# Performance work log

Hardware: AMD Instinct MI355X
Metric: run time of the kernel (lower is better)

The kernel has to match this reference:

```python
import jax, jax.numpy as jnp
import numpy as np
from jax import lax

DN = ('NCHW', 'OIHW', 'NCHW')


def conv2d(x, w, b, stride, pad):
    y = lax.conv_general_dilated(x, w, (stride, stride), [(pad, pad), (pad, pad)],
                                 dimension_numbers=DN)
    return y + b[None, :, None, None]


def conv_transpose2d_k4s2p1(x, w, b):
    # torch ConvTranspose2d(k=4, s=2, p=1); w is torch layout [Cin, Cout, 4, 4].
    # Equivalent forward conv: lhs_dilation=2, pad = k-1-p = 2, spatially-flipped kernel.
    k = jnp.flip(w, (2, 3)).transpose(1, 0, 2, 3)  # -> OIHW [Cout, Cin, 4, 4]
    y = lax.conv_general_dilated(x, k, (1, 1), [(2, 2), (2, 2)],
                                 lhs_dilation=(2, 2), dimension_numbers=DN)
    return y + b[None, :, None, None]


def setup_inputs() -> dict:
    key = jax.random.key(0)
    ks = jax.random.split(key, 16)

    def w(k, shape):
        fan_in = int(np.prod(shape[1:]))
        return jax.random.normal(k, shape, jnp.float32) * np.float32(1.0 / np.sqrt(fan_in))

    inp = {}
    inp['x'] = jax.random.uniform(ks[0], (256, 1, 128, 128), jnp.float32)
    # Encoder
    inp['enc_w1'] = w(ks[1], (32, 1, 4, 4));   inp['enc_b1'] = jnp.zeros((32,), jnp.float32)
    inp['enc_w2'] = w(ks[2], (64, 32, 4, 4));  inp['enc_b2'] = jnp.zeros((64,), jnp.float32)
    inp['enc_w3'] = w(ks[3], (64, 64, 3, 3));  inp['enc_b3'] = jnp.zeros((64,), jnp.float32)
    inp['enc_w4'] = w(ks[4], (32, 64, 1, 1));  inp['enc_b4'] = jnp.zeros((32,), jnp.float32)
    # Codebook: uniform(-sqrt(3/512), sqrt(3/512))
    mx = np.float32(np.sqrt(3.0 / 512.0))
    inp['codebook'] = jax.random.uniform(ks[5], (512, 32), jnp.float32, -mx, mx)
    # Decoder
    inp['dec_w1'] = w(ks[6], (64, 32, 3, 3));  inp['dec_b1'] = jnp.zeros((64,), jnp.float32)
    inp['dect_w1'] = w(ks[7], (64, 32, 4, 4)); inp['dect_b1'] = jnp.zeros((32,), jnp.float32)  # torch [Cin,Cout,k,k]
    inp['dect_w2'] = w(ks[8], (32, 1, 4, 4));  inp['dect_b2'] = jnp.zeros((1,), jnp.float32)
    return inp


def vqvae_forward(x, enc_w1, enc_b1, enc_w2, enc_b2, enc_w3, enc_b3, enc_w4, enc_b4,
                  codebook, dec_w1, dec_b1, dect_w1, dect_b1, dect_w2, dect_b2):
    # Encoder: 128 -> 64 -> 32 spatial, 32 channels out
    h = jax.nn.relu(conv2d(x, enc_w1, enc_b1, 2, 1))
    h = jax.nn.relu(conv2d(h, enc_w2, enc_b2, 2, 1))
    h = jax.nn.relu(conv2d(h, enc_w3, enc_b3, 1, 1))
    z = conv2d(h, enc_w4, enc_b4, 1, 0)            # [B, 32, 32, 32]

    # Vector quantization (NCHW -> NHWC -> flat)
    zin = jnp.moveaxis(z, 1, -1)                   # [B, H, W, D]
    flat = zin.reshape(-1, zin.shape[-1])          # [N, D]
    dists = (jnp.sum(flat * flat, -1, keepdims=True)
             + jnp.sum(codebook * codebook, -1)
             - 2.0 * flat @ codebook.T)            # [N, K]
    idx = jnp.argmin(dists, -1)                    # [N]
    quant = codebook[idx].reshape(zin.shape)       # == one_hot @ codebook

    emb_loss = jnp.mean((quant - lax.stop_gradient(zin)) ** 2)
    com_loss = 0.26 * jnp.mean((lax.stop_gradient(quant) - zin) ** 2)
    vq_loss = emb_loss + com_loss
    quant = zin + lax.stop_gradient(quant - zin)   # straight-through
    qz = jnp.moveaxis(quant, -1, 1)                # [B, 32, 32, 32]

    # Decoder: 32 -> 64 -> 128 spatial
    d = jax.nn.relu(conv2d(qz, dec_w1, dec_b1, 1, 1))
    d = jax.nn.relu(conv_transpose2d_k4s2p1(d, dect_w1, dect_b1))
    recon = jax.nn.sigmoid(conv_transpose2d_k4s2p1(d, dect_w2, dect_b2))
    return recon, vq_loss


def reference(x, enc_w1, enc_b1, enc_w2, enc_b2, enc_w3, enc_b3, enc_w4, enc_b4,
              codebook, dec_w1, dec_b1, dect_w1, dect_b1, dect_w2, dect_b2):
    return vqvae_forward(x, enc_w1, enc_b1, enc_w2, enc_b2, enc_w3, enc_b3, enc_w4, enc_b4,
                         codebook, dec_w1, dec_b1, dect_w1, dect_b1, dect_w2, dect_b2)
```

## Files before the change

kernel.cpp:

```cpp
#include <hip/hip_runtime.h>
#include <math.h>

typedef __attribute__((ext_vector_type(8))) short short8;
typedef __attribute__((ext_vector_type(4))) float f32x4;

__device__ inline unsigned short f2bf(float f) {
  unsigned u = __float_as_uint(f);
  u = (u + 0x7fffu + ((u >> 16) & 1u)) >> 16;
  return (unsigned short)u;
}

__global__ __launch_bounds__(256, 4)
void conv1_lds(const float* __restrict__ x, const float* __restrict__ w,
               const float* __restrict__ bias, float* __restrict__ out) {
  int bid = blockIdx.x;
  int cchunk = bid & 1;
  int t4 = (bid >> 1) & 3;
  int n = bid >> 3;
  int co0 = cchunk * 16;
  int y0 = t4 * 16;
  int yi0 = 2 * y0 - 1;

  __shared__ float xs[34 * 128];
  __shared__ float wl[16][16];

  int t = threadIdx.x;
  for (int idx = t; idx < 34 * 128; idx += 256) {
    int gy = yi0 + (idx >> 7);
    int gx = idx & 127;
    bool ok = (unsigned)gy < 128;
    xs[idx] = ok ? x[(size_t)n * 16384 + gy * 128 + gx] : 0.f;
  }
  {
    int cc = t & 15;
    int tap = t >> 4;
    if (t < 256) wl[tap][cc] = w[(size_t)(co0 + cc) * 16 + tap];
  }
  __syncthreads();

  int sx = t & 63;
  int rg = t >> 6;

  float acc[4][16];
#pragma unroll
  for (int j = 0; j < 4; j++)
#pragma unroll
    for (int c = 0; c < 16; c++) acc[j][c] = 0.f;

  int ix0 = 2 * sx - 1;
#pragma unroll
  for (int ky = 0; ky < 4; ky++) {
#pragma unroll
    for (int kx = 0; kx < 4; kx++) {
      int ix = ix0 + kx;
      bool xok = (unsigned)ix < 128;
      float xv[4];
#pragma unroll
      for (int j = 0; j < 4; j++) {
        int lrow = 2 * (4 * rg + j) + ky;
        float v = xs[lrow * 128 + (xok ? ix : 0)];
        xv[j] = xok ? v : 0.f;
      }
      const float* wr = &wl[ky * 4 + kx][0];
#pragma unroll
      for (int c = 0; c < 16; c += 4) {
        float4 wv = *(const float4*)(wr + c);
#pragma unroll
        for (int j = 0; j < 4; j++) {
          acc[j][c + 0] = fmaf(xv[j], wv.x, acc[j][c + 0]);
          acc[j][c + 1] = fmaf(xv[j], wv.y, acc[j][c + 1]);
          acc[j][c + 2] = fmaf(xv[j], wv.z, acc[j][c + 2]);
          acc[j][c + 3] = fmaf(xv[j], wv.w, acc[j][c + 3]);
        }
      }
    }
  }

#pragma unroll
  for (int j = 0; j < 4; j++) {
    int oy = y0 + 4 * rg + j;
    float* op = out + (((size_t)n * 32 + co0) * 64 + oy) * 64 + sx;
#pragma unroll
    for (int c = 0; c < 16; c++) {
      float v = acc[j][c] + bias[co0 + c];
      op[(size_t)c * 4096] = fmaxf(v, 0.f);
    }
  }
}

template<int CIN, int COUT, int CCH>
__global__ __launch_bounds__(256, 4)
void conv4x4s2_p(const float* __restrict__ x, const float* __restrict__ w,
                 const float* __restrict__ bias, float* __restrict__ out) {
  constexpr int NCH = COUT / CCH;
  int bid = blockIdx.x;
  int cchunk = bid % NCH;
  int n = bid / NCH;
  int co0 = cchunk * CCH;

  __shared__ float xs[66 * 68];
  __shared__ float wl[16][CCH];

  int t = threadIdx.x;
  int sx = t & 31;
  int sy0 = t >> 5;

  for (int i = t; i < 66 * 68; i += 256) xs[i] = 0.f;

  float acc[4][CCH];
#pragma unroll
  for (int j = 0; j < 4; j++)
#pragma unroll
    for (int c = 0; c < CCH; c++) acc[j][c] = 0.f;

  const float* xn = x + (size_t)n * CIN * 4096;

  for (int ci = 0; ci < CIN; ci++) {
    __syncthreads();
#pragma unroll
    for (int k = 0; k < 4; k++) {
      int idx = k * 1024 + t * 4;
      int row = idx >> 6;
      int col = idx & 63;
      float4 v = *(const float4*)(xn + (size_t)ci * 4096 + idx);
      float* rp = xs + (row + 1) * 68;
      int h = col >> 1;
      rp[34 + h]     = v.x;
      rp[h + 1]      = v.y;
      rp[34 + h + 1] = v.z;
      rp[h + 2]      = v.w;
    }
    {
      int cc = t & (CCH - 1);
      int tap = t >> 4;
      if (tap < 16) wl[tap][cc] = w[(size_t)(co0 + cc) * (CIN * 16) + ci * 16 + tap];
    }
    __syncthreads();

#pragma unroll
    for (int ky = 0; ky < 4; ky++) {
#pragma unroll
      for (int kx = 0; kx < 4; kx++) {
        int pc = ((kx & 1) ? 34 : 0) + sx + (kx >> 1);
        float xv[4];
#pragma unroll
        for (int j = 0; j < 4; j++) {
          int row = 2 * (sy0 + j * 8) + ky;
          xv[j] = xs[row * 68 + pc];
        }
        const float* wr = &wl[ky * 4 + kx][0];
#pragma unroll
        for (int c = 0; c < CCH; c += 4) {
          float4 wv = *(const float4*)(wr + c);
#pragma unroll
          for (int j = 0; j < 4; j++) {
            acc[j][c + 0] = fmaf(xv[j], wv.x, acc[j][c + 0]);
            acc[j][c + 1] = fmaf(xv[j], wv.y, acc[j][c + 1]);
            acc[j][c + 2] = fmaf(xv[j], wv.z, acc[j][c + 2]);
            acc[j][c + 3] = fmaf(xv[j], wv.w, acc[j][c + 3]);
          }
        }
      }
    }
  }

#pragma unroll
  for (int j = 0; j < 4; j++) {
    int sy = sy0 + j * 8;
    float* op = out + (((size_t)n * COUT + co0) * 32 + sy) * 32 + sx;
#pragma unroll
    for (int c = 0; c < CCH; c++) {
      float v = acc[j][c] + bias[co0 + c];
      v = fmaxf(v, 0.f);
      op[(size_t)c * 1024] = v;
    }
  }
}

template<int CIN, int COUT>
__global__ __launch_bounds__(256, 3)
void conv3x3_r8(const float* __restrict__ x, const float* __restrict__ w,
                const float* __restrict__ bias, float* __restrict__ out) {
  constexpr int NCH = COUT / 16;
  int bid = blockIdx.x;
  int cchunk = bid % NCH;
  int n = bid / NCH;
  int co0 = cchunk * 16;

  __shared__ float xs[4 * 34 * 34];
  __shared__ float wl[4 * 9][16];

  int t = threadIdx.x;
  int sx = t & 31;
  int rg = (t >> 5) & 3;
  int cob = (t >> 7) * 8;

  for (int i = t; i < 4 * 34 * 34; i += 256) xs[i] = 0.f;

  float acc[8][8];
#pragma unroll
  for (int j = 0; j < 8; j++)
#pragma unroll
    for (int c = 0; c < 8; c++) acc[j][c] = 0.f;

  const float* xn = x + (size_t)n * CIN * 1024;

  for (int cg = 0; cg < CIN / 4; cg++) {
    __syncthreads();
#pragma unroll
    for (int k = 0; k < 4; k++) {
      int row = t >> 3;
      int col = (t & 7) * 4;
      float4 v = *(const float4*)(xn + (size_t)(cg * 4 + k) * 1024 + t * 4);
      float* dst = xs + k * 1156 + (row + 1) * 34 + col + 1;
      dst[0] = v.x; dst[1] = v.y; dst[2] = v.z; dst[3] = v.w;
    }
    for (int i = t; i < 4 * 9 * 16; i += 256) {
      int cc = i & 15;
      int row = i >> 4;
      int c4 = row / 9, kk = row % 9;
      wl[row][cc] = w[(size_t)(co0 + cc) * (CIN * 9) + (cg * 4 + c4) * 9 + kk];
    }
    __syncthreads();

#pragma unroll
    for (int c4 = 0; c4 < 4; c4++) {
      const float* xc = xs + c4 * 1156;
      float xv[10][3];
#pragma unroll
      for (int r = 0; r < 10; r++) {
#pragma unroll
        for (int cx = 0; cx < 3; cx++)
          xv[r][cx] = xc[(8 * rg + r) * 34 + sx + cx];
      }
#pragma unroll
      for (int ky = 0; ky < 3; ky++) {
#pragma unroll
        for (int kx = 0; kx < 3; kx++) {
          const float* wr = &wl[c4 * 9 + ky * 3 + kx][cob];
          float4 w0 = *(const float4*)(wr);
          float4 w1 = *(const float4*)(wr + 4);
#pragma unroll
          for (int j = 0; j < 8; j++) {
            float xx = xv[j + ky][kx];
            acc[j][0] = fmaf(xx, w0.x, acc[j][0]);
            acc[j][1] = fmaf(xx, w0.y, acc[j][1]);
            acc[j][2] = fmaf(xx, w0.z, acc[j][2]);
            acc[j][3] = fmaf(xx, w0.w, acc[j][3]);
            acc[j][4] = fmaf(xx, w1.x, acc[j][4]);
            acc[j][5] = fmaf(xx, w1.y, acc[j][5]);
            acc[j][6] = fmaf(xx, w1.z, acc[j][6]);
            acc[j][7] = fmaf(xx, w1.w, acc[j][7]);
          }
        }
      }
    }
  }

#pragma unroll
  for (int j = 0; j < 8; j++) {
    int sy = 8 * rg + j;
    float* op = out + (((size_t)n * COUT + co0 + cob) * 32 + sy) * 32 + sx;
#pragma unroll
    for (int c = 0; c < 8; c++) {
      float v = acc[j][c] + bias[co0 + cob + c];
      v = fmaxf(v, 0.f);
      op[(size_t)c * 1024] = v;
    }
  }
}

__global__ void wprep_dect1(const float* __restrict__ tw1,
                            unsigned short* __restrict__ Bws) {
  int i = blockIdx.x * 256 + threadIdx.x;
  if (i < 32768) {
    int ci = i & 63;
    int co = (i >> 6) & 31;
    int tap = (i >> 11) & 3;
    int par = i >> 13;
    int py = par >> 1, px = par & 1;
    int ky0 = (py + 1) & 1, kx0 = (px + 1) & 1;
    int kyi = tap >> 1, kxi = tap & 1;
    int ky = ky0 + 2 * kyi, kx = kx0 + 2 * kxi;
    Bws[i] = f2bf(tw1[(((size_t)ci * 32 + co) * 4 + ky) * 4 + kx]);
  }
}

__global__ void wprep_dec1(const float* __restrict__ dw1,
                           unsigned short* __restrict__ Wd1) {
  int i = blockIdx.x * 256 + threadIdx.x;
  if (i < 18432) {
    int ci = i & 31;
    int tap = (i >> 5) % 9;
    int co = i / 288;
    Wd1[i] = f2bf(dw1[(size_t)(co * 32 + ci) * 9 + tap]);
  }
}

__global__ __launch_bounds__(256, 4)
void dec1_mfma(const float* __restrict__ qz,
               const unsigned short* __restrict__ Wd1,
               const float* __restrict__ bias, float* __restrict__ d1) {
  int strip = blockIdx.x & 3;
  int smp = blockIdx.x >> 2;
  int y0 = strip * 8;

  __shared__ __align__(16) unsigned short xt[10 * 34 * 32];

  int t = threadIdx.x;
  for (int idx = t; idx < 16 * 10 * 34; idx += 256) {
    int cc = idx % 34;
    int tmp = idx / 34;
    int rr = tmp % 10;
    int pp = tmp / 10;
    int gy = y0 - 1 + rr;
    int gx = cc - 1;
    bool ok = ((unsigned)gy < 32) && ((unsigned)gx < 32);
    const float* p = qz + ((size_t)smp * 32 + 2 * pp) * 1024 + gy * 32 + gx;
    float v0 = ok ? p[0] : 0.f;
    float v1 = ok ? p[1024] : 0.f;
    unsigned pk = (unsigned)f2bf(v0) | ((unsigned)f2bf(v1) << 16);
    *(unsigned*)(&xt[(rr * 34 + cc) * 32 + 2 * pp]) = pk;
  }

  int lane = t & 63;
  int wv = t >> 6;
  int mlo = lane & 15;
  int khi = lane >> 4;

  short8 afr[9];
#pragma unroll
  for (int tap = 0; tap < 9; tap++)
    afr[tap] = *(const short8*)(Wd1 + (size_t)(wv * 16 + mlo) * 288 +
                                tap * 32 + khi * 8);
  float bb[4];
#pragma unroll
  for (int r = 0; r < 4; r++) bb[r] = bias[wv * 16 + khi * 4 + r];

  __syncthreads();

  for (int pt = 0; pt < 16; pt++) {
    int rl = pt >> 1;
    int chf = pt & 1;
    f32x4 acc = {0.f, 0.f, 0.f, 0.f};
#pragma unroll
    for (int tap = 0; tap < 9; tap++) {
      int ky = tap / 3, kx = tap % 3;
      const unsigned short* bp =
          xt + (((rl + ky) * 34) + chf * 16 + mlo + kx) * 32 + khi * 8;
      short8 b = *(const short8*)bp;
      acc = __builtin_amdgcn_mfma_f32_16x16x32_bf16(afr[tap], b, acc, 0, 0, 0);
    }
    int gyo = y0 + rl;
    int gxo = chf * 16 + mlo;
#pragma unroll
    for (int r = 0; r < 4; r++) {
      int co = wv * 16 + khi * 4 + r;
      d1[(((size_t)smp * 64 + co) * 32 + gyo) * 32 + gxo] =
          fmaxf(acc[r] + bb[r], 0.f);
    }
  }
}

__global__ __launch_bounds__(256, 4)
void convt_mfma(const float* __restrict__ d1,
                const unsigned short* __restrict__ Bws,
                const float* __restrict__ bias, float* __restrict__ d2) {
  constexpr int CP = 72;
  int bid = blockIdx.x;
  int rp = bid & 15;
  int smp = bid >> 4;

  __shared__ __align__(16) unsigned short xt[4 * 34 * CP];

  int t = threadIdx.x;

  for (int idx = t; idx < 32 * 4 * 34; idx += 256) {
    int cc = idx % 34;
    int tmp = idx / 34;
    int rr = tmp & 3;
    int pp = tmp >> 2;
    int gy = 2 * rp - 1 + rr;
    int gx = cc - 1;
    bool ok = ((unsigned)gy < 32) && ((unsigned)gx < 32);
    const float* p = d1 + ((size_t)smp * 64 + 2 * pp) * 1024 + gy * 32 + gx;
    float v0 = ok ? p[0] : 0.f;
    float v1 = ok ? p[1024] : 0.f;
    unsigned pk = (unsigned)f2bf(v0) | ((unsigned)f2bf(v1) << 16);
    *(unsigned*)(&xt[(rr * 34 + cc) * CP + 2 * pp]) = pk;
  }
  __syncthreads();

  int lane = t & 63;
  int wv = t >> 6;
  int row2 = wv >> 1;
  int c0 = (wv & 1) * 16;
  int mlo = lane & 15;
  int khi = lane >> 4;

  f32x4 acc[4][2];
#pragma unroll
  for (int par = 0; par < 4; par++)
#pragma unroll
    for (int nt = 0; nt < 2; nt++) {
      f32x4 z = {0.f, 0.f, 0.f, 0.f};
      acc[par][nt] = z;
    }

#pragma unroll
  for (int par = 0; par < 4; par++) {
    int py = par >> 1, px = par & 1;
    int ky0 = (py + 1) & 1, kx0 = (px + 1) & 1;
    int ay = (py + 1 - ky0) >> 1;
    int ax = (px + 1 - kx0) >> 1;
#pragma unroll
    for (int tap = 0; tap < 4; tap++) {
      int kyi = tap >> 1, kxi = tap & 1;
      int rrp = row2 + 1 + (ay - kyi);
      int ccb = c0 + 1 + (ax - kxi);
#pragma unroll
      for (int kc = 0; kc < 2; kc++) {
        const unsigned short* ap =
            xt + ((rrp * 34) + ccb + mlo) * CP + kc * 32 + khi * 8;
        short8 a = *(const short8*)ap;
#pragma unroll
        for (int nt = 0; nt < 2; nt++) {
          const unsigned short* bp =
              Bws + (((size_t)(par * 4 + tap) * 32 + nt * 16 + mlo) * 64) +
              kc * 32 + khi * 8;
          short8 b = *(const short8*)bp;
          acc[par][nt] =
              __builtin_amdgcn_mfma_f32_16x16x32_bf16(a, b, acc[par][nt], 0, 0, 0);
        }
      }
    }
  }

  int sy = 2 * rp + row2;
#pragma unroll
  for (int par = 0; par < 4; par++) {
    int py = par >> 1, px = par & 1;
    int oy = 2 * sy + py;
#pragma unroll
    for (int nt = 0; nt < 2; nt++) {
      int co = nt * 16 + mlo;
      float b = bias[co];
      float* op = d2 + (((size_t)smp * 32 + co) * 64 + oy) * 64;
#pragma unroll
      for (int r = 0; r < 4; r++) {
        int sx = c0 + khi * 4 + r;
        int ox = 2 * sx + px;
        op[ox] = fmaxf(acc[par][nt][r] + b, 0.f);
      }
    }
  }
}

__global__ __launch_bounds__(256, 4)
void dect2_full(const float* __restrict__ x, const float* __restrict__ w,
                const float* __restrict__ bias, float* __restrict__ out) {
  int ptile = blockIdx.x & 3;
  int n = blockIdx.x >> 2;
  int y0 = ptile * 16;

  __shared__ float xs[8][1152];
  int t = threadIdx.x;
  int sx = t & 63;
  int r4 = t >> 6;

  float acc[4][4];
#pragma unroll
  for (int j = 0; j < 4; j++)
#pragma unroll
    for (int p = 0; p < 4; p++) acc[j][p] = 0.f;

  const float* xn = x + (size_t)n * 32 * 4096;

  for (int cg = 0; cg < 4; cg++) {
    __syncthreads();
    for (int idx = t; idx < 8 * 1152; idx += 256) {
      int ch = idx / 1152;
      int rem = idx % 1152;
      int iy = y0 - 1 + rem / 64;
      int ix = rem & 63;
      bool ok = (unsigned)iy < 64;
      xs[ch][rem] = ok ? xn[(size_t)(cg * 8 + ch) * 4096 + iy * 64 + ix] : 0.f;
    }
    __syncthreads();

#pragma unroll
    for (int c4 = 0; c4 < 8; c4++) {
      int ci = cg * 8 + c4;
      const float* xc = &xs[c4][0];
      float xv[6][3];
#pragma unroll
      for (int r = 0; r < 6; r++) {
        int srow = 4 * r4 + r;
#pragma unroll
        for (int cx = 0; cx < 3; cx++) {
          int ix = sx - 1 + cx;
          bool ok = (unsigned)ix < 64;
          float v = xc[ok ? srow * 64 + ix : 0];
          xv[r][cx] = ok ? v : 0.f;
        }
      }
      float w16[16];
#pragma unroll
      for (int q = 0; q < 4; q++) {
        float4 ww = *(const float4*)(w + ci * 16 + 4 * q);
        w16[4 * q + 0] = ww.x; w16[4 * q + 1] = ww.y;
        w16[4 * q + 2] = ww.z; w16[4 * q + 3] = ww.w;
      }
#pragma unroll
      for (int py = 0; py < 2; py++) {
#pragma unroll
        for (int px = 0; px < 2; px++) {
          int par = py * 2 + px;
          int ky0 = (py + 1) & 1, kx0 = (px + 1) & 1;
          int ay = (py + 1 - ky0) >> 1;
          int ax = (px + 1 - kx0) >> 1;
#pragma unroll
          for (int kyi = 0; kyi < 2; kyi++) {
#pragma unroll
            for (int kxi = 0; kxi < 2; kxi++) {
              float wv = w16[(ky0 + 2 * kyi) * 4 + (kx0 + 2 * kxi)];
#pragma unroll
              for (int j = 0; j < 4; j++) {
                float xx = xv[j + ay + 1 - kyi][ax + 1 - kxi];
                acc[j][par] = fmaf(xx, wv, acc[j][par]);
              }
            }
          }
        }
      }
    }
  }

  float b0 = bias[0];
#pragma unroll
  for (int j = 0; j < 4; j++) {
    int iy = y0 + 4 * r4 + j;
#pragma unroll
    for (int py = 0; py < 2; py++) {
      float v0 = acc[j][py * 2 + 0] + b0;
      float v1 = acc[j][py * 2 + 1] + b0;
      float2 o;
      o.x = 1.f / (1.f + expf(-v0));
      o.y = 1.f / (1.f + expf(-v1));
      int oy = 2 * iy + py;
      *(float2*)(out + (size_t)n * 16384 + oy * 128 + 2 * sx) = o;
    }
  }
}

__global__ void cbn_prep(const float* __restrict__ cb, float* __restrict__ cbn) {
#pragma clang fp contract(off)
  int k = blockIdx.x * 256 + threadIdx.x;
  if (k < 512) {
    float m[32];
#pragma unroll
    for (int d = 0; d < 32; d++) {
      float c = cb[k * 32 + d];
      m[d] = c * c;
    }
    float r[8];
#pragma unroll
    for (int j = 0; j < 8; j++)
      r[j] = ((m[j] + m[8 + j]) + m[16 + j]) + m[24 + j];
    cbn[k] = ((r[0] + r[1]) + (r[2] + r[3])) + ((r[4] + r[5]) + (r[6] + r[7]));
  }
}

__global__ __launch_bounds__(256)
void vq_fused(const float* __restrict__ h3, const float* __restrict__ w4,
              const float* __restrict__ b4, const float* __restrict__ cb,
              const float* __restrict__ cbn, float* __restrict__ qz,
              float* __restrict__ loss) {
  __shared__ float wl[64][32];
  int tid = threadIdx.x;
  for (int i = tid; i < 2048; i += 256) {
    int co = i & 31;
    int ci = i >> 5;
    wl[ci][co] = w4[(size_t)co * 64 + ci];
  }
  __syncthreads();

  int n = blockIdx.x >> 2;
  int p = (blockIdx.x & 3) * 256 + tid;
  const float* hn = h3 + (size_t)n * 65536;

  float zv[32];
#pragma unroll
  for (int c = 0; c < 32; c++) zv[c] = 0.f;
  for (int ci = 0; ci < 64; ci++) {
    float xv = hn[(size_t)ci * 1024 + p];
#pragma unroll
    for (int c = 0; c < 32; c += 4) {
      float4 wv = *(const float4*)&wl[ci][c];
      zv[c + 0] = fmaf(xv, wv.x, zv[c + 0]);
      zv[c + 1] = fmaf(xv, wv.y, zv[c + 1]);
      zv[c + 2] = fmaf(xv, wv.z, zv[c + 2]);
      zv[c + 3] = fmaf(xv, wv.w, zv[c + 3]);
    }
  }
#pragma unroll
  for (int c = 0; c < 32; c++) zv[c] = zv[c] + b4[c];

  float zz;
  {
#pragma clang fp contract(off)
    float m[32];
#pragma unroll
    for (int d = 0; d < 32; d++) m[d] = zv[d] * zv[d];
    float r[8];
#pragma unroll
    for (int j = 0; j < 8; j++)
      r[j] = ((m[j] + m[8 + j]) + m[16 + j]) + m[24 + j];
    zz = ((r[0] + r[1]) + (r[2] + r[3])) + ((r[4] + r[5]) + (r[6] + r[7]));
  }

  float best = 3.4e38f;
  int bk = 0;
  for (int k4 = 0; k4 < 512; k4 += 4) {
    float4 cn = *(const float4*)(cbn + k4);
    float da[4];
#pragma unroll
    for (int u = 0; u < 4; u++) da[u] = 0.f;
#pragma unroll
    for (int d = 0; d < 32; d += 4) {
#pragma unroll
      for (int u = 0; u < 4; u++) {
        float4 c = *(const float4*)(cb + (size_t)(k4 + u) * 32 + d);
        float a = da[u];
        a = fmaf(zv[d + 0], c.x, a);
        a = fmaf(zv[d + 1], c.y, a);
        a = fmaf(zv[d + 2], c.z, a);
        a = fmaf(zv[d + 3], c.w, a);
        da[u] = a;
      }
    }
#pragma unroll
    for (int u = 0; u < 4; u++) {
      float cnu = (u == 0) ? cn.x : (u == 1) ? cn.y : (u == 2) ? cn.z : cn.w;
      float s;
      {
#pragma clang fp contract(off)
        s = (zz + cnu) - 2.f * da[u];
      }
      int k = k4 + u;
      if (s < best) { best = s; bk = k; }
    }
  }

  float lsum = 0.f;
  float* qn = qz + (size_t)n * 32768;
#pragma unroll
  for (int d = 0; d < 32; d += 4) {
#pragma clang fp contract(off)
    float4 q = *(const float4*)(cb + (size_t)bk * 32 + d);
    float e;
    e = q.x - zv[d + 0]; lsum = fmaf(e, e, lsum);
    e = q.y - zv[d + 1]; lsum = fmaf(e, e, lsum);
    e = q.z - zv[d + 2]; lsum = fmaf(e, e, lsum);
    e = q.w - zv[d + 3]; lsum = fmaf(e, e, lsum);
    qn[(size_t)(d + 0) * 1024 + p] = zv[d + 0] + (q.x - zv[d + 0]);
    qn[(size_t)(d + 1) * 1024 + p] = zv[d + 1] + (q.y - zv[d + 1]);
    qn[(size_t)(d + 2) * 1024 + p] = zv[d + 2] + (q.z - zv[d + 2]);
    qn[(size_t)(d + 3) * 1024 + p] = zv[d + 3] + (q.w - zv[d + 3]);
  }

#pragma unroll
  for (int off = 32; off; off >>= 1) lsum += __shfl_down(lsum, off, 64);
  if ((tid & 63) == 0) atomicAdd(loss, lsum);
}

__global__ void finalize_loss(const float* __restrict__ loss, float* __restrict__ out) {
  if (threadIdx.x == 0) {
    float m = loss[0] / 8388608.f;
    out[0] = m + 0.26f * m;
  }
}

extern "C" void kernel_launch(void* const* d_in, const int* in_sizes, int n_in,
                              void* d_out, int out_size, void* d_ws, size_t ws_size,
                              hipStream_t stream) {
  (void)in_sizes; (void)n_in; (void)out_size;
  const float* x   = (const float*)d_in[0];
  const float* ew1 = (const float*)d_in[1];
  const float* eb1 = (const float*)d_in[2];
  const float* ew2 = (const float*)d_in[3];
  const float* eb2 = (const float*)d_in[4];
  const float* ew3 = (const float*)d_in[5];
  const float* eb3 = (const float*)d_in[6];
  const float* ew4 = (const float*)d_in[7];
  const float* eb4 = (const float*)d_in[8];
  const float* cb  = (const float*)d_in[9];
  const float* dw1 = (const float*)d_in[10];
  const float* db1 = (const float*)d_in[11];
  const float* tw1 = (const float*)d_in[12];
  const float* tb1 = (const float*)d_in[13];
  const float* tw2 = (const float*)d_in[14];
  const float* tb2 = (const float*)d_in[15];
  float* out = (float*)d_out;

  auto need = [](size_t c) -> size_t {
    return (c * 196608 + 516 + 16384 + 9216) * 4;
  };
  int nchunks = 4;
  if (ws_size >= need(256)) nchunks = 1;
  else if (ws_size >= need(128)) nchunks = 2;
  int chunk = 256 / nchunks;

  float* ws = (float*)d_ws;
  float* A = ws;
  float* B = A + (size_t)chunk * 131072;
  float* cbn = B + (size_t)chunk * 65536;
  float* lossacc = cbn + 512;
  unsigned short* Bws = (unsigned short*)(cbn + 516);
  unsigned short* Wd1 = (unsigned short*)(cbn + 516 + 16384);

  float* h1 = A;
  float* h2 = B;
  float* h3 = A;
  float* qz = A + (size_t)chunk * 98304;
  float* d1 = B;
  float* d2 = A;

  cbn_prep<<<2, 256, 0, stream>>>(cb, cbn);
  wprep_dect1<<<128, 256, 0, stream>>>(tw1, Bws);
  wprep_dec1<<<72, 256, 0, stream>>>(dw1, Wd1);
  (void)hipMemsetAsync(lossacc, 0, 4, stream);

  for (int c = 0; c < nchunks; c++) {
    const float* xc = x + (size_t)c * chunk * 128 * 128;
    float* outc = out + (size_t)c * chunk * 128 * 128;

    conv1_lds<<<chunk * 8, 256, 0, stream>>>(xc, ew1, eb1, h1);
    conv4x4s2_p<32, 64, 16>
        <<<chunk * 4, 256, 0, stream>>>(h1, ew2, eb2, h2);
    conv3x3_r8<64, 64>
        <<<chunk * 4, 256, 0, stream>>>(h2, ew3, eb3, h3);

    vq_fused<<<chunk * 4, 256, 0, stream>>>(h3, ew4, eb4, cb, cbn, qz, lossacc);

    dec1_mfma<<<chunk * 4, 256, 0, stream>>>(qz, Wd1, db1, d1);
    convt_mfma<<<chunk * 16, 256, 0, stream>>>(d1, Bws, tb1, d2);
    dect2_full<<<chunk * 4, 256, 0, stream>>>(d2, tw2, tb2, outc);
  }

  finalize_loss<<<1, 64, 0, stream>>>(lossacc, out + 4194304);
}
```

Baseline: 1.039 ms.

## Double-buffer enc3 conv3x3 with async global-to-LDS loads and prepacked weights

Rewrites the 3x3 encoder conv to double-buffer its input and weight tiles in LDS. It fills them with global_load_lds async copies so the next channel group loads while the current one computes. Weights are prepacked once by a new kernel into a per-block contiguous layout. The padded LDS tile is dropped in favour of bounds-checked reads, which adds per-element predication, and launch bounds are raised to 4 blocks per CU. LDS doubles (about 37KB), which may limit occupancy. The sync placement relies on the async loads being complete at the barrier, and there is no explicit vmcnt wait.

```diff
diff --git a/kernel.cpp b/kernel.cpp
--- a/kernel.cpp
+++ b/kernel.cpp
@@ -8,6 +8,17 @@
   unsigned u = __float_as_uint(f);
   u = (u + 0x7fffu + ((u >> 16) & 1u)) >> 16;
   return (unsigned short)u;
+}
+
+__device__ inline void async16(const float* g, float* l) {
+  __builtin_amdgcn_global_load_lds(
+      (const __attribute__((address_space(1))) void*)g,
+      (__attribute__((address_space(3))) void*)l, 16, 0, 0);
+}
+__device__ inline void async4(const float* g, float* l) {
+  __builtin_amdgcn_global_load_lds(
+      (const __attribute__((address_space(1))) void*)g,
+      (__attribute__((address_space(3))) void*)l, 4, 0, 0);
 }
 
 __global__ __launch_bounds__(256, 4)
@@ -177,9 +188,22 @@
   }
 }
 
+__global__ void wprep_enc3p(const float* __restrict__ w, float* __restrict__ wt) {
+  int i = blockIdx.x * 256 + threadIdx.x;
+  if (i < 36864) {
+    int cc = i & 15;
+    int row = (i >> 4) % 36;
+    int blk = i / 576;
+    int cch = blk & 3;
+    int cg = blk >> 2;
+    int c4 = row / 9, kk = row % 9;
+    wt[i] = w[(size_t)(cch * 16 + cc) * (64 * 9) + (cg * 4 + c4) * 9 + kk];
+  }
+}
+
 template<int CIN, int COUT>
-__global__ __launch_bounds__(256, 3)
-void conv3x3_r8(const float* __restrict__ x, const float* __restrict__ w,
+__global__ __launch_bounds__(256, 4)
+void conv3x3_db(const float* __restrict__ x, const float* __restrict__ wp,
                 const float* __restrict__ bias, float* __restrict__ out) {
   constexpr int NCH = COUT / 16;
   int bid = blockIdx.x;
@@ -187,15 +211,17 @@
   int n = bid / NCH;
   int co0 = cchunk * 16;
 
-  __shared__ float xs[4 * 34 * 34];
-  __shared__ float wl[4 * 9][16];
+  __shared__ float xs[2][4][1024];
+  __shared__ float wl[2][36][16];
 
   int t = threadIdx.x;
+  int lane = t & 63;
+  int wv = t >> 6;
   int sx = t & 31;
   int rg = (t >> 5) & 3;
   int cob = (t >> 7) * 8;
 
-  for (int i = t; i < 4 * 34 * 34; i += 256) xs[i] = 0.f;
+  const float* xn = x + (size_t)n * CIN * 1024;
 
   float acc[8][8];
 #pragma unroll
@@ -203,41 +229,52 @@
 #pragma unroll
     for (int c = 0; c < 8; c++) acc[j][c] = 0.f;
 
-  const float* xn = x + (size_t)n * CIN * 1024;
-
+  auto stage = [&](int buf, int cg) {
+    const float* src = xn + (size_t)cg * 4096;
+    float* db = &xs[buf][0][0];
+#pragma unroll
+    for (int c = 0; c < 4; c++) {
+      int chunk = wv * 4 + c;
+      async16(src + chunk * 256 + lane * 4, db + chunk * 256);
+    }
+    const float* wsrc = wp + (size_t)(cg * NCH + cchunk) * 576;
+    float* wb = &wl[buf][0][0];
+#pragma unroll
+    for (int c = 0; c < 3; c++) {
+      int chunk = wv + c * 4;
+      if (chunk < 9)
+        async4(wsrc + chunk * 64 + lane, wb + chunk * 64);
+    }
+  };
+
+  stage(0, 0);
+  __syncthreads();
+
+  int cur = 0;
   for (int cg = 0; cg < CIN / 4; cg++) {
-    __syncthreads();
-#pragma unroll
-    for (int k = 0; k < 4; k++) {
-      int row = t >> 3;
-      int col = (t & 7) * 4;
-      float4 v = *(const float4*)(xn + (size_t)(cg * 4 + k) * 1024 + t * 4);
-      float* dst = xs + k * 1156 + (row + 1) * 34 + col + 1;
-      dst[0] = v.x; dst[1] = v.y; dst[2] = v.z; dst[3] = v.w;
-    }
-    for (int i = t; i < 4 * 9 * 16; i += 256) {
-      int cc = i & 15;
-      int row = i >> 4;
-      int c4 = row / 9, kk = row % 9;
-      wl[row][cc] = w[(size_t)(co0 + cc) * (CIN * 9) + (cg * 4 + c4) * 9 + kk];
-    }
-    __syncthreads();
+    if (cg + 1 < CIN / 4) stage(cur ^ 1, cg + 1);
 
 #pragma unroll
     for (int c4 = 0; c4 < 4; c4++) {
-      const float* xc = xs + c4 * 1156;
+      const float* xc = &xs[cur][c4][0];
       float xv[10][3];
 #pragma unroll
       for (int r = 0; r < 10; r++) {
-#pragma unroll
-        for (int cx = 0; cx < 3; cx++)
-          xv[r][cx] = xc[(8 * rg + r) * 34 + sx + cx];
+        int iy = 8 * rg - 1 + r;
+        bool yok = (unsigned)iy < 32;
+#pragma unroll
+        for (int cx = 0; cx < 3; cx++) {
+          int ix = sx - 1 + cx;
+          bool ok = yok && ((unsigned)ix < 32);
+          float v = xc[ok ? iy * 32 + ix : 0];
+          xv[r][cx] = ok ? v : 0.f;
+        }
       }
 #pragma unroll
       for (int ky = 0; ky < 3; ky++) {
 #pragma unroll
         for (int kx = 0; kx < 3; kx++) {
-          const float* wr = &wl[c4 * 9 + ky * 3 + kx][cob];
+          const float* wr = &wl[cur][c4 * 9 + ky * 3 + kx][cob];
           float4 w0 = *(const float4*)(wr);
           float4 w1 = *(const float4*)(wr + 4);
 #pragma unroll
@@ -255,6 +292,8 @@
         }
       }
     }
+    __syncthreads();
+    cur ^= 1;
   }
 
 #pragma unroll
@@ -704,7 +743,7 @@
   float* out = (float*)d_out;
 
   auto need = [](size_t c) -> size_t {
-    return (c * 196608 + 516 + 16384 + 9216) * 4;
+    return (c * 196608 + 516 + 16384 + 9216 + 36864) * 4;
   };
   int nchunks = 4;
   if (ws_size >= need(256)) nchunks = 1;
@@ -718,6 +757,7 @@
   float* lossacc = cbn + 512;
   unsigned short* Bws = (unsigned short*)(cbn + 516);
   unsigned short* Wd1 = (unsigned short*)(cbn + 516 + 16384);
+  float* We3p = cbn + 516 + 16384 + 9216;
 
   float* h1 = A;
   float* h2 = B;
@@ -729,6 +769,7 @@
   cbn_prep<<<2, 256, 0, stream>>>(cb, cbn);
   wprep_dect1<<<128, 256, 0, stream>>>(tw1, Bws);
   wprep_dec1<<<72, 256, 0, stream>>>(dw1, Wd1);
+  wprep_enc3p<<<144, 256, 0, stream>>>(ew3, We3p);
   (void)hipMemsetAsync(lossacc, 0, 4, stream);
 
   for (int c = 0; c < nchunks; c++) {
@@ -738,8 +779,8 @@
     conv1_lds<<<chunk * 8, 256, 0, stream>>>(xc, ew1, eb1, h1);
     conv4x4s2_p<32, 64, 16>
         <<<chunk * 4, 256, 0, stream>>>(h1, ew2, eb2, h2);
-    conv3x3_r8<64, 64>
-        <<<chunk * 4, 256, 0, stream>>>(h2, ew3, eb3, h3);
+    conv3x3_db<64, 64>
+        <<<chunk * 4, 256, 0, stream>>>(h2, We3p, eb3, h3);
 
     vq_fused<<<chunk * 4, 256, 0, stream>>>(h3, ew4, eb4, cb, cbn, qz, lossacc);
 
```

Result: slower. 1.177 ms (+13.4%).
